# Optimization experiments

Hardware: AMD Instinct MI355X
Metric: run time of the kernel (lower is better)

Reference implementation:

```python
import jax, jax.numpy as jnp
import numpy as np

B, T, D, H = 4096, 512, 8, 64  # batch, seq_len, input_size, hidden_size


def setup_inputs() -> dict:
    key = jax.random.key(0)
    ks = jax.random.split(key, 11)
    s = lambda k, shape: (jax.random.normal(k, shape, dtype=jnp.float32) * 0.1)
    return {
        "x": jax.random.normal(ks[0], (B, T, D), dtype=jnp.float32),
        # layer 0 (input_size -> H), PyTorch gate order i,f,g,o packed along 4H
        "Wih0": s(ks[1], (4 * H, D)),
        "Whh0": s(ks[2], (4 * H, H)),
        "bih0": s(ks[3], (4 * H,)),
        "bhh0": s(ks[4], (4 * H,)),
        # layer 1 (H -> H)
        "Wih1": s(ks[5], (4 * H, H)),
        "Whh1": s(ks[6], (4 * H, H)),
        "bih1": s(ks[7], (4 * H,)),
        "bhh1": s(ks[8], (4 * H,)),
        # final linear head H -> 1
        "Wfc": s(ks[9], (1, H)),
        "bfc": s(ks[10], (1,)),
    }


def _lstm_layer(x, Wih, Whh, bih, bhh):
    """Single-direction LSTM layer over x:[B,T,Din] -> hs:[B,T,H]."""
    b, t, _ = x.shape
    h_dim = Whh.shape[1]
    # Precompute input contribution for all timesteps (one big GEMM).
    xg = jnp.einsum("btd,gd->btg", x, Wih) + bih + bhh  # [B,T,4H]

    def step(carry, gx_t):
        h, c = carry
        z = gx_t + h @ Whh.T  # [B,4H]
        i, f, g, o = jnp.split(z, 4, axis=-1)
        i = jax.nn.sigmoid(i)
        f = jax.nn.sigmoid(f)
        g = jnp.tanh(g)
        o = jax.nn.sigmoid(o)
        c = f * c + i * g
        h = o * jnp.tanh(c)
        return (h, c), h

    h0 = jnp.zeros((b, h_dim), x.dtype)
    c0 = jnp.zeros((b, h_dim), x.dtype)
    (_, _), hs = jax.lax.scan(step, (h0, c0), jnp.swapaxes(xg, 0, 1))
    return jnp.swapaxes(hs, 0, 1)  # [B,T,H]


def reference(x, Wih0, Whh0, bih0, bhh0, Wih1, Whh1, bih1, bhh1, Wfc, bfc):
    # nn.LSTM with num_layers=2, batch_first=True; dropout inactive in eval.
    h1 = _lstm_layer(x, Wih0, Whh0, bih0, bhh0)
    h2 = _lstm_layer(h1, Wih1, Whh1, bih1, bhh1)
    last = h2[:, -1, :]  # [B,H]
    return last @ Wfc.T + bfc  # [B,1]
```

## Files before the change

### kernel.cpp

```cpp
#include <hip/hip_runtime.h>

#define BTOT 4096
#define TB   512
#define BD   8
#define BSL  16
#define K0   96
#define K0E  104
#define K1   128
#define K1E  136

typedef __attribute__((ext_vector_type(8))) short  short8;
typedef __attribute__((ext_vector_type(4))) float  f32x4;

static __device__ __forceinline__ unsigned short f2bf(float f) {
    unsigned u = __float_as_uint(f);
    u += 0x7fffu + ((u >> 16) & 1u);
    return (unsigned short)(u >> 16);
}
static __device__ __forceinline__ float bf2f(unsigned short h) {
    return __uint_as_float(((unsigned)h) << 16);
}
static __device__ __forceinline__ float sigm(float x) {
    float e = __builtin_amdgcn_exp2f(-1.44269504f * x);
    return __builtin_amdgcn_rcpf(1.0f + e);
}
static __device__ __forceinline__ float tanh_(float x) {
    float e = __builtin_amdgcn_exp2f(2.88539008f * x);
    return 1.0f - 2.0f * __builtin_amdgcn_rcpf(1.0f + e);
}

__global__ __launch_bounds__(512, 2) void lstm2_fused(
    const float* __restrict__ x,
    const float* __restrict__ Wih0, const float* __restrict__ Whh0,
    const float* __restrict__ bih0, const float* __restrict__ bhh0,
    const float* __restrict__ Wih1, const float* __restrict__ Whh1,
    const float* __restrict__ bih1, const float* __restrict__ bhh1,
    const float* __restrict__ Wfc,  const float* __restrict__ bfc,
    float* __restrict__ out)
{
    __shared__ __align__(16) unsigned short A0[2][BSL][K0E];
    __shared__ __align__(16) unsigned short A1[2][BSL][K1E];

    const int tid  = threadIdx.x;
    const int wid  = tid >> 6;
    const int lane = tid & 63;
    const int q    = lane >> 4;
    const int ln   = lane & 15;
    const int rb   = blockIdx.x * BSL;

    const bool L1w = (wid >= 4);
    const int  g   = L1w ? (wid - 4) : wid;
    const int  jc  = g * 16 + ln;

    short8 Bf[4][4];
    #pragma unroll
    for (int G = 0; G < 4; ++G) {
        const int n = G * 64 + jc;
        #pragma unroll
        for (int ki = 0; ki < 4; ++ki) {
            union { unsigned short u[8]; short8 v; } t;
            #pragma unroll
            for (int j = 0; j < 8; ++j) {
                const int k = ki * 32 + q * 8 + j;
                float w = 0.0f;
                if (!L1w) {
                    if (ki < 3) {
                        if (k < 64)      w = Whh0[n * 64 + k];
                        else if (k < 72) w = Wih0[n * 8 + (k - 64)];
                    }
                } else {
                    if (k < 64)          w = Wih1[n * 64 + k];
                    else                 w = Whh1[n * 64 + (k - 64)];
                }
                t.u[j] = f2bf(w);
            }
            Bf[G][ki] = t.v;
        }
    }
    float bias[4];
    #pragma unroll
    for (int G = 0; G < 4; ++G) {
        const int n = G * 64 + jc;
        bias[G] = L1w ? (bih1[n] + bhh1[n]) : (bih0[n] + bhh0[n]);
    }

    {
        unsigned short* p0 = &A0[0][0][0];
        for (int i = tid; i < 2 * BSL * K0E; i += 512) p0[i] = 0;
        unsigned short* p1 = &A1[0][0][0];
        for (int i = tid; i < 2 * BSL * K1E; i += 512) p1[i] = 0;
    }
    __syncthreads();
    if (!L1w && lane < 8) {
        const int xrow = g * 4 + (lane >> 1), xh = lane & 1;
        const float4 v = *(const float4*)(x + ((size_t)(rb + xrow) * TB) * BD + xh * 4);
        unsigned long long pk =
            (unsigned long long)f2bf(v.x)        |
            ((unsigned long long)f2bf(v.y) << 16) |
            ((unsigned long long)f2bf(v.z) << 32) |
            ((unsigned long long)f2bf(v.w) << 48);
        *(unsigned long long*)&A0[0][xrow][64 + xh * 4] = pk;
    }
    __syncthreads();

    float cc[4] = {0.f, 0.f, 0.f, 0.f};

    for (int it = 0; it <= TB; ++it) {
        if (!L1w) {
            const int t = it;
            if (t < TB) {
                float4 xv;
                const bool dox = (lane < 8) && (t + 1 < TB);
                const int xrow = g * 4 + (lane >> 1), xh = lane & 1;
                if (dox)
                    xv = *(const float4*)(x + ((size_t)(rb + xrow) * TB + (t + 1)) * BD + xh * 4);

                const unsigned short* Ar = &A0[t & 1][ln][0];
                const short8 a0 = *(const short8*)(Ar + 0 * 32 + q * 8);
                const short8 a1 = *(const short8*)(Ar + 1 * 32 + q * 8);
                const short8 a2 = *(const short8*)(Ar + 2 * 32 + q * 8);

                f32x4 ai = {0.f,0.f,0.f,0.f}, af = ai, ag = ai, ao = ai;
                ai = __builtin_amdgcn_mfma_f32_16x16x32_bf16(a0, Bf[0][0], ai, 0, 0, 0);
                af = __builtin_amdgcn_mfma_f32_16x16x32_bf16(a0, Bf[1][0], af, 0, 0, 0);
                ag = __builtin_amdgcn_mfma_f32_16x16x32_bf16(a0, Bf[2][0], ag, 0, 0, 0);
                ao = __builtin_amdgcn_mfma_f32_16x16x32_bf16(a0, Bf[3][0], ao, 0, 0, 0);
                ai = __builtin_amdgcn_mfma_f32_16x16x32_bf16(a1, Bf[0][1], ai, 0, 0, 0);
                af = __builtin_amdgcn_mfma_f32_16x16x32_bf16(a1, Bf[1][1], af, 0, 0, 0);
                ag = __builtin_amdgcn_mfma_f32_16x16x32_bf16(a1, Bf[2][1], ag, 0, 0, 0);
                ao = __builtin_amdgcn_mfma_f32_16x16x32_bf16(a1, Bf[3][1], ao, 0, 0, 0);
                ai = __builtin_amdgcn_mfma_f32_16x16x32_bf16(a2, Bf[0][2], ai, 0, 0, 0);
                af = __builtin_amdgcn_mfma_f32_16x16x32_bf16(a2, Bf[1][2], af, 0, 0, 0);
                ag = __builtin_amdgcn_mfma_f32_16x16x32_bf16(a2, Bf[2][2], ag, 0, 0, 0);
                ao = __builtin_amdgcn_mfma_f32_16x16x32_bf16(a2, Bf[3][2], ao, 0, 0, 0);

                #pragma unroll
                for (int r = 0; r < 4; ++r) {
                    const float iv = sigm (ai[r] + bias[0]);
                    const float fv = sigm (af[r] + bias[1]);
                    const float gv = tanh_(ag[r] + bias[2]);
                    const float ov = sigm (ao[r] + bias[3]);
                    cc[r] = fv * cc[r] + iv * gv;
                    const float hv = ov * tanh_(cc[r]);
                    const unsigned short hb = f2bf(hv);
                    const int br = q * 4 + r;
                    A0[(t + 1) & 1][br][jc] = hb;
                    A1[t & 1][br][jc]       = hb;
                }
                if (dox) {
                    unsigned long long pk =
                        (unsigned long long)f2bf(xv.x)        |
                        ((unsigned long long)f2bf(xv.y) << 16) |
                        ((unsigned long long)f2bf(xv.z) << 32) |
                        ((unsigned long long)f2bf(xv.w) << 48);
                    *(unsigned long long*)&A0[(t + 1) & 1][xrow][64 + xh * 4] = pk;
                }
            }
        } else {
            const int t1 = it - 1;
            if (t1 >= 0) {
                const unsigned short* Ar = &A1[t1 & 1][ln][0];
                const short8 a0 = *(const short8*)(Ar + 0 * 32 + q * 8);
                const short8 a1 = *(const short8*)(Ar + 1 * 32 + q * 8);
                const short8 a2 = *(const short8*)(Ar + 2 * 32 + q * 8);
                const short8 a3 = *(const short8*)(Ar + 3 * 32 + q * 8);

                f32x4 ai = {0.f,0.f,0.f,0.f}, af = ai, ag = ai, ao = ai;
                ai = __builtin_amdgcn_mfma_f32_16x16x32_bf16(a0, Bf[0][0], ai, 0, 0, 0);
                af = __builtin_amdgcn_mfma_f32_16x16x32_bf16(a0, Bf[1][0], af, 0, 0, 0);
                ag = __builtin_amdgcn_mfma_f32_16x16x32_bf16(a0, Bf[2][0], ag, 0, 0, 0);
                ao = __builtin_amdgcn_mfma_f32_16x16x32_bf16(a0, Bf[3][0], ao, 0, 0, 0);
                ai = __builtin_amdgcn_mfma_f32_16x16x32_bf16(a1, Bf[0][1], ai, 0, 0, 0);
                af = __builtin_amdgcn_mfma_f32_16x16x32_bf16(a1, Bf[1][1], af, 0, 0, 0);
                ag = __builtin_amdgcn_mfma_f32_16x16x32_bf16(a1, Bf[2][1], ag, 0, 0, 0);
                ao = __builtin_amdgcn_mfma_f32_16x16x32_bf16(a1, Bf[3][1], ao, 0, 0, 0);
                ai = __builtin_amdgcn_mfma_f32_16x16x32_bf16(a2, Bf[0][2], ai, 0, 0, 0);
                af = __builtin_amdgcn_mfma_f32_16x16x32_bf16(a2, Bf[1][2], af, 0, 0, 0);
                ag = __builtin_amdgcn_mfma_f32_16x16x32_bf16(a2, Bf[2][2], ag, 0, 0, 0);
                ao = __builtin_amdgcn_mfma_f32_16x16x32_bf16(a2, Bf[3][2], ao, 0, 0, 0);
                ai = __builtin_amdgcn_mfma_f32_16x16x32_bf16(a3, Bf[0][3], ai, 0, 0, 0);
                af = __builtin_amdgcn_mfma_f32_16x16x32_bf16(a3, Bf[1][3], af, 0, 0, 0);
                ag = __builtin_amdgcn_mfma_f32_16x16x32_bf16(a3, Bf[2][3], ag, 0, 0, 0);
                ao = __builtin_amdgcn_mfma_f32_16x16x32_bf16(a3, Bf[3][3], ao, 0, 0, 0);

                #pragma unroll
                for (int r = 0; r < 4; ++r) {
                    const float iv = sigm (ai[r] + bias[0]);
                    const float fv = sigm (af[r] + bias[1]);
                    const float gv = tanh_(ag[r] + bias[2]);
                    const float ov = sigm (ao[r] + bias[3]);
                    cc[r] = fv * cc[r] + iv * gv;
                    const float hv = ov * tanh_(cc[r]);
                    const int br = q * 4 + r;
                    A1[(t1 + 1) & 1][br][64 + jc] = f2bf(hv);
                }
            }
        }
        __syncthreads();
    }

    if (tid < BSL) {
        float s = bfc[0];
        #pragma unroll 8
        for (int j = 0; j < 64; ++j)
            s += bf2f(A1[0][tid][64 + j]) * Wfc[j];
        out[rb + tid] = s;
    }
}

extern "C" void kernel_launch(void* const* d_in, const int* in_sizes, int n_in,
                              void* d_out, int out_size, void* d_ws, size_t ws_size,
                              hipStream_t stream) {
    const float* x    = (const float*)d_in[0];
    const float* Wih0 = (const float*)d_in[1];
    const float* Whh0 = (const float*)d_in[2];
    const float* bih0 = (const float*)d_in[3];
    const float* bhh0 = (const float*)d_in[4];
    const float* Wih1 = (const float*)d_in[5];
    const float* Whh1 = (const float*)d_in[6];
    const float* bih1 = (const float*)d_in[7];
    const float* bhh1 = (const float*)d_in[8];
    const float* Wfc  = (const float*)d_in[9];
    const float* bfc  = (const float*)d_in[10];
    float* out = (float*)d_out;

    dim3 grid(BTOT / BSL);
    dim3 block(512);
    lstm2_fused<<<grid, block, 0, stream>>>(x, Wih0, Whh0, bih0, bhh0,
                                            Wih1, Whh1, bih1, bhh1, Wfc, bfc, out);
}
```

Before: 579.6 us.

## Double waves per block to split gate math, fold bias into MFMA accumulators

Doubles the block to 1024 threads (16 waves), so each layer uses 8 waves. Each wave still computes the full MFMA tile but evaluates the gate nonlinearities for only two of its four accumulator rows, which shortens the serial activation chain per timestep. The change also seeds the MFMA accumulators with the bias, packs bf16 conversions with v_cvt_pk_bf16_f32, and replaces indexed double buffers with precomputed LDS offsets toggled by XOR. The cost is duplicated MFMA work, twice the register pressure per block, and a barrier across more waves at every step.

```diff
diff --git a/kernel.cpp b/kernel.cpp
--- a/kernel.cpp
+++ b/kernel.cpp
@@ -4,10 +4,13 @@
 #define TB   512
 #define BD   8
 #define BSL  16
-#define K0   96
-#define K0E  104
-#define K1   128
-#define K1E  136
+
+#define A0P1   2048
+#define A1P0   8192
+#define A1XOR  4096
+#define S0     104
+#define S1     136
+#define LDSEL  16384
 
 typedef __attribute__((ext_vector_type(8))) short  short8;
 typedef __attribute__((ext_vector_type(4))) float  f32x4;
@@ -29,7 +32,30 @@
     return 1.0f - 2.0f * __builtin_amdgcn_rcpf(1.0f + e);
 }
 
-__global__ __launch_bounds__(512, 2) void lstm2_fused(
+template<int R0>
+static __device__ __forceinline__ unsigned gates2(
+    const f32x4 ai, const f32x4 af, const f32x4 ag, const f32x4 ao,
+    float& c0, float& c1)
+{
+    float h0, h1;
+    {
+        const float iv = sigm(ai[R0]),     fv = sigm(af[R0]);
+        const float gv = tanh_(ag[R0]),    ov = sigm(ao[R0]);
+        c0 = fv * c0 + iv * gv;
+        h0 = ov * tanh_(c0);
+    }
+    {
+        const float iv = sigm(ai[R0 + 1]), fv = sigm(af[R0 + 1]);
+        const float gv = tanh_(ag[R0 + 1]), ov = sigm(ao[R0 + 1]);
+        c1 = fv * c1 + iv * gv;
+        h1 = ov * tanh_(c1);
+    }
+    unsigned hp;
+    asm("v_cvt_pk_bf16_f32 %0, %1, %2" : "=v"(hp) : "v"(h0), "v"(h1));
+    return hp;
+}
+
+__global__ __launch_bounds__(1024) void lstm2_fused(
     const float* __restrict__ x,
     const float* __restrict__ Wih0, const float* __restrict__ Whh0,
     const float* __restrict__ bih0, const float* __restrict__ bhh0,
@@ -38,8 +64,7 @@
     const float* __restrict__ Wfc,  const float* __restrict__ bfc,
     float* __restrict__ out)
 {
-    __shared__ __align__(16) unsigned short A0[2][BSL][K0E];
-    __shared__ __align__(16) unsigned short A1[2][BSL][K1E];
+    __shared__ __align__(16) unsigned short lds16[LDSEL];
 
     const int tid  = threadIdx.x;
     const int wid  = tid >> 6;
@@ -48,8 +73,11 @@
     const int ln   = lane & 15;
     const int rb   = blockIdx.x * BSL;
 
-    const bool L1w = (wid >= 4);
-    const int  g   = L1w ? (wid - 4) : wid;
+    const bool L1w = (wid >= 8);
+    const int  w   = L1w ? (wid - 8) : wid;
+    const int  g   = w & 3;
+    const int  rh  = w >> 2;
+    const int  r0  = rh * 2;
     const int  jc  = g * 16 + ln;
 
     short8 Bf[4][4];
@@ -62,17 +90,17 @@
             #pragma unroll
             for (int j = 0; j < 8; ++j) {
                 const int k = ki * 32 + q * 8 + j;
-                float w = 0.0f;
+                float wv = 0.0f;
                 if (!L1w) {
                     if (ki < 3) {
-                        if (k < 64)      w = Whh0[n * 64 + k];
-                        else if (k < 72) w = Wih0[n * 8 + (k - 64)];
+                        if (k < 64)      wv = Whh0[n * 64 + k];
+                        else if (k < 72) wv = Wih0[n * 8 + (k - 64)];
                     }
                 } else {
-                    if (k < 64)          w = Wih1[n * 64 + k];
-                    else                 w = Whh1[n * 64 + (k - 64)];
+                    if (k < 64)          wv = Wih1[n * 64 + k];
+                    else                 wv = Whh1[n * 64 + (k - 64)];
                 }
-                t.u[j] = f2bf(w);
+                t.u[j] = f2bf(wv);
             }
             Bf[G][ki] = t.v;
         }
@@ -85,42 +113,53 @@
     }
 
     {
-        unsigned short* p0 = &A0[0][0][0];
-        for (int i = tid; i < 2 * BSL * K0E; i += 512) p0[i] = 0;
-        unsigned short* p1 = &A1[0][0][0];
-        for (int i = tid; i < 2 * BSL * K1E; i += 512) p1[i] = 0;
+        unsigned* z = (unsigned*)lds16;
+        #pragma unroll
+        for (int i = 0; i < 8; ++i) z[tid + i * 1024] = 0;
     }
     __syncthreads();
-    if (!L1w && lane < 8) {
-        const int xrow = g * 4 + (lane >> 1), xh = lane & 1;
+
+    const int xrow = g * 4 + (lane >> 1), xh = lane & 1;
+    if (!L1w && rh == 0 && lane < 8) {
         const float4 v = *(const float4*)(x + ((size_t)(rb + xrow) * TB) * BD + xh * 4);
-        unsigned long long pk =
-            (unsigned long long)f2bf(v.x)        |
-            ((unsigned long long)f2bf(v.y) << 16) |
-            ((unsigned long long)f2bf(v.z) << 32) |
-            ((unsigned long long)f2bf(v.w) << 48);
-        *(unsigned long long*)&A0[0][xrow][64 + xh * 4] = pk;
+        unsigned p0, p1;
+        asm("v_cvt_pk_bf16_f32 %0, %1, %2" : "=v"(p0) : "v"(v.x), "v"(v.y));
+        asm("v_cvt_pk_bf16_f32 %0, %1, %2" : "=v"(p1) : "v"(v.z), "v"(v.w));
+        *(uint2*)(lds16 + (xrow * S0 + 64 + xh * 4)) = make_uint2(p0, p1);
     }
     __syncthreads();
 
-    float cc[4] = {0.f, 0.f, 0.f, 0.f};
+    int rdA, wrA, wrC = 0, wrX = 0, xrA, xrW;
+    if (!L1w) {
+        rdA = ln * S0 + q * 8;
+        wrA = A0P1 + (q * 4 + r0) * S0 + jc;
+        wrC = A1P0 + (q * 4 + r0) * S1 + jc;
+        wrX = A0P1 + xrow * S0 + 64 + xh * 4;
+        xrA = A0P1; xrW = A0P1;
+    } else {
+        rdA = A1P0 + A1XOR + ln * S1 + q * 8;
+        wrA = A1P0 + (q * 4 + r0) * S1 + 64 + jc;
+        xrA = A1XOR; xrW = A1XOR;
+    }
+
+    float cc0 = 0.f, cc1 = 0.f;
 
     for (int it = 0; it <= TB; ++it) {
         if (!L1w) {
-            const int t = it;
-            if (t < TB) {
+            if (it < TB) {
                 float4 xv;
-                const bool dox = (lane < 8) && (t + 1 < TB);
-                const int xrow = g * 4 + (lane >> 1), xh = lane & 1;
+                const bool dox = (rh == 0) && (lane < 8) && (it + 1 < TB);
                 if (dox)
-                    xv = *(const float4*)(x + ((size_t)(rb + xrow) * TB + (t + 1)) * BD + xh * 4);
-
-                const unsigned short* Ar = &A0[t & 1][ln][0];
-                const short8 a0 = *(const short8*)(Ar + 0 * 32 + q * 8);
-                const short8 a1 = *(const short8*)(Ar + 1 * 32 + q * 8);
-                const short8 a2 = *(const short8*)(Ar + 2 * 32 + q * 8);
-
-                f32x4 ai = {0.f,0.f,0.f,0.f}, af = ai, ag = ai, ao = ai;
+                    xv = *(const float4*)(x + ((size_t)(rb + xrow) * TB + (it + 1)) * BD + xh * 4);
+
+                const short8 a0 = *(const short8*)(lds16 + rdA);
+                const short8 a1 = *(const short8*)(lds16 + rdA + 32);
+                const short8 a2 = *(const short8*)(lds16 + rdA + 64);
+
+                f32x4 ai = {bias[0], bias[0], bias[0], bias[0]};
+                f32x4 af = {bias[1], bias[1], bias[1], bias[1]};
+                f32x4 ag = {bias[2], bias[2], bias[2], bias[2]};
+                f32x4 ao = {bias[3], bias[3], bias[3], bias[3]};
                 ai = __builtin_amdgcn_mfma_f32_16x16x32_bf16(a0, Bf[0][0], ai, 0, 0, 0);
                 af = __builtin_amdgcn_mfma_f32_16x16x32_bf16(a0, Bf[1][0], af, 0, 0, 0);
                 ag = __builtin_amdgcn_mfma_f32_16x16x32_bf16(a0, Bf[2][0], ag, 0, 0, 0);
@@ -134,38 +173,31 @@
                 ag = __builtin_amdgcn_mfma_f32_16x16x32_bf16(a2, Bf[2][2], ag, 0, 0, 0);
                 ao = __builtin_amdgcn_mfma_f32_16x16x32_bf16(a2, Bf[3][2], ao, 0, 0, 0);
 
-                #pragma unroll
-                for (int r = 0; r < 4; ++r) {
-                    const float iv = sigm (ai[r] + bias[0]);
-                    const float fv = sigm (af[r] + bias[1]);
-                    const float gv = tanh_(ag[r] + bias[2]);
-                    const float ov = sigm (ao[r] + bias[3]);
-                    cc[r] = fv * cc[r] + iv * gv;
-                    const float hv = ov * tanh_(cc[r]);
-                    const unsigned short hb = f2bf(hv);
-                    const int br = q * 4 + r;
-                    A0[(t + 1) & 1][br][jc] = hb;
-                    A1[t & 1][br][jc]       = hb;
-                }
+                const unsigned hp = rh ? gates2<2>(ai, af, ag, ao, cc0, cc1)
+                                       : gates2<0>(ai, af, ag, ao, cc0, cc1);
+                lds16[wrA]      = (unsigned short)hp;
+                lds16[wrA + S0] = (unsigned short)(hp >> 16);
+                lds16[wrC]      = (unsigned short)hp;
+                lds16[wrC + S1] = (unsigned short)(hp >> 16);
+
                 if (dox) {
-                    unsigned long long pk =
-                        (unsigned long long)f2bf(xv.x)        |
-                        ((unsigned long long)f2bf(xv.y) << 16) |
-                        ((unsigned long long)f2bf(xv.z) << 32) |
-                        ((unsigned long long)f2bf(xv.w) << 48);
-                    *(unsigned long long*)&A0[(t + 1) & 1][xrow][64 + xh * 4] = pk;
+                    unsigned p0, p1;
+                    asm("v_cvt_pk_bf16_f32 %0, %1, %2" : "=v"(p0) : "v"(xv.x), "v"(xv.y));
+                    asm("v_cvt_pk_bf16_f32 %0, %1, %2" : "=v"(p1) : "v"(xv.z), "v"(xv.w));
+                    *(uint2*)(lds16 + wrX) = make_uint2(p0, p1);
                 }
             }
         } else {
-            const int t1 = it - 1;
-            if (t1 >= 0) {
-                const unsigned short* Ar = &A1[t1 & 1][ln][0];
-                const short8 a0 = *(const short8*)(Ar + 0 * 32 + q * 8);
-                const short8 a1 = *(const short8*)(Ar + 1 * 32 + q * 8);
-                const short8 a2 = *(const short8*)(Ar + 2 * 32 + q * 8);
-                const short8 a3 = *(const short8*)(Ar + 3 * 32 + q * 8);
-
-                f32x4 ai = {0.f,0.f,0.f,0.f}, af = ai, ag = ai, ao = ai;
+            if (it >= 1) {
+                const short8 a0 = *(const short8*)(lds16 + rdA);
+                const short8 a1 = *(const short8*)(lds16 + rdA + 32);
+                const short8 a2 = *(const short8*)(lds16 + rdA + 64);
+                const short8 a3 = *(const short8*)(lds16 + rdA + 96);
+
+                f32x4 ai = {bias[0], bias[0], bias[0], bias[0]};
+                f32x4 af = {bias[1], bias[1], bias[1], bias[1]};
+                f32x4 ag = {bias[2], bias[2], bias[2], bias[2]};
+                f32x4 ao = {bias[3], bias[3], bias[3], bias[3]};
                 ai = __builtin_amdgcn_mfma_f32_16x16x32_bf16(a0, Bf[0][0], ai, 0, 0, 0);
                 af = __builtin_amdgcn_mfma_f32_16x16x32_bf16(a0, Bf[1][0], af, 0, 0, 0);
                 ag = __builtin_amdgcn_mfma_f32_16x16x32_bf16(a0, Bf[2][0], ag, 0, 0, 0);
@@ -183,27 +215,21 @@
                 ag = __builtin_amdgcn_mfma_f32_16x16x32_bf16(a3, Bf[2][3], ag, 0, 0, 0);
                 ao = __builtin_amdgcn_mfma_f32_16x16x32_bf16(a3, Bf[3][3], ao, 0, 0, 0);
 
-                #pragma unroll
-                for (int r = 0; r < 4; ++r) {
-                    const float iv = sigm (ai[r] + bias[0]);
-                    const float fv = sigm (af[r] + bias[1]);
-                    const float gv = tanh_(ag[r] + bias[2]);
-                    const float ov = sigm (ao[r] + bias[3]);
-                    cc[r] = fv * cc[r] + iv * gv;
-                    const float hv = ov * tanh_(cc[r]);
-                    const int br = q * 4 + r;
-                    A1[(t1 + 1) & 1][br][64 + jc] = f2bf(hv);
-                }
+                const unsigned hp = rh ? gates2<2>(ai, af, ag, ao, cc0, cc1)
+                                       : gates2<0>(ai, af, ag, ao, cc0, cc1);
+                lds16[wrA]      = (unsigned short)hp;
+                lds16[wrA + S1] = (unsigned short)(hp >> 16);
             }
         }
         __syncthreads();
+        rdA ^= xrA; wrA ^= xrW; wrC ^= A1XOR; wrX ^= A0P1;
     }
 
     if (tid < BSL) {
         float s = bfc[0];
         #pragma unroll 8
         for (int j = 0; j < 64; ++j)
-            s += bf2f(A1[0][tid][64 + j]) * Wfc[j];
+            s += bf2f(lds16[A1P0 + tid * S1 + 64 + j]) * Wfc[j];
         out[rb + tid] = s;
     }
 }
@@ -225,7 +251,7 @@
     float* out = (float*)d_out;
 
     dim3 grid(BTOT / BSL);
-    dim3 block(512);
+    dim3 block(1024);
     lstm2_fused<<<grid, block, 0, stream>>>(x, Wih0, Whh0, bih0, bhh0,
                                             Wih1, Whh1, bih1, bhh1, Wfc, bfc, out);
 }
```

New measurement: 607.5 us. 4.8% more time.
